# Optimization experiments

Measured on AMD Instinct MI355X. Metric: run time of the kernel, lower is better.

## Reference

```python
import jax, jax.numpy as jnp
import numpy as np
from jax import lax

H = 1024
NH = 16
R = 32
B, S = 32, 1024
LN_EPS = 1e-5

def _gelu(x):
    return jax.nn.gelu(x, approximate=False)

def setup_inputs() -> dict:
    key = jax.random.key(0)
    ks = jax.random.split(key, 24)
    w = lambda k, shape: jax.random.normal(k, shape, jnp.float32) * 0.02
    d = {}
    d['computation_results'] = jax.random.normal(ks[0], (B, S, H), jnp.float32)
    d['max_steps'] = 16
    # rule selector: Linear(H,H), GELU, Linear(H,R)
    d['rule_w1'] = w(ks[1], (H, H)); d['rule_b1'] = jnp.zeros((H,))
    d['rule_w2'] = w(ks[2], (R, H)); d['rule_b2'] = jnp.zeros((R,))
    d['rule_emb'] = jax.random.normal(ks[3], (R, H), jnp.float32)
    # MultiheadAttention packed in-proj [3H,H] and out-proj [H,H]
    d['attn_in_w'] = w(ks[4], (3 * H, H)); d['attn_in_b'] = jnp.zeros((3 * H,))
    d['attn_out_w'] = w(ks[5], (H, H)); d['attn_out_b'] = jnp.zeros((H,))
    # 2-layer LSTM, PyTorch gate order i,f,g,o
    d['lstm_wih0'] = w(ks[6], (4 * H, H)); d['lstm_whh0'] = w(ks[7], (4 * H, H))
    d['lstm_bih0'] = jnp.zeros((4 * H,)); d['lstm_bhh0'] = jnp.zeros((4 * H,))
    d['lstm_wih1'] = w(ks[8], (4 * H, H)); d['lstm_whh1'] = w(ks[9], (4 * H, H))
    d['lstm_bih1'] = jnp.zeros((4 * H,)); d['lstm_bhh1'] = jnp.zeros((4 * H,))
    # step generator: Linear(H,2H), LayerNorm(2H), GELU, Linear(2H,H)
    d['gen_w1'] = w(ks[10], (2 * H, H)); d['gen_b1'] = jnp.zeros((2 * H,))
    d['gen_ln_g'] = jnp.ones((2 * H,)); d['gen_ln_b'] = jnp.zeros((2 * H,))
    d['gen_w2'] = w(ks[11], (H, 2 * H)); d['gen_b2'] = jnp.zeros((H,))
    # step validator: Linear(2H,H), GELU, Linear(H,1), Sigmoid
    d['val_w1'] = w(ks[12], (H, 2 * H)); d['val_b1'] = jnp.zeros((H,))
    d['val_w2'] = w(ks[13], (1, H)); d['val_b2'] = jnp.zeros((1,))
    # proof verifier: Linear(H,H), GELU, Linear(H,1), Sigmoid
    d['ver_w1'] = w(ks[14], (H, H)); d['ver_b1'] = jnp.zeros((H,))
    d['ver_w2'] = w(ks[15], (1, H)); d['ver_b2'] = jnp.zeros((1,))
    return d


def reference(computation_results, max_steps, rule_w1, rule_b1, rule_w2, rule_b2, rule_emb,
              attn_in_w, attn_in_b, attn_out_w, attn_out_b,
              lstm_wih0, lstm_whh0, lstm_bih0, lstm_bhh0,
              lstm_wih1, lstm_whh1, lstm_bih1, lstm_bhh1,
              gen_w1, gen_b1, gen_ln_g, gen_ln_b, gen_w2, gen_b2,
              val_w1, val_b1, val_w2, val_b2,
              ver_w1, ver_b1, ver_w2, ver_b2):
    comp = computation_results
    b, s, h = comp.shape
    dh = h // NH
    scale = dh ** -0.5
    wq, wk, wv = jnp.split(attn_in_w, 3, axis=0)
    bq, bk, bv = jnp.split(attn_in_b, 3, axis=0)
    # K/V projections of the static context, computed once outside the step loop
    K = (comp @ wk.T + bk).reshape(b, s, NH, dh)  # [B,S,NH,dh]
    V = (comp @ wv.T + bv).reshape(b, s, NH, dh)
    lstm_params = ((lstm_wih0, lstm_whh0, lstm_bih0, lstm_bhh0),
                   (lstm_wih1, lstm_whh1, lstm_bih1, lstm_bhh1))

    def step(carry, _):
        ps, hmem, cmem = carry  # ps: [B,H]; hmem/cmem: [2,B,H]
        # rule selection
        logits = _gelu(ps @ rule_w1.T + rule_b1) @ rule_w2.T + rule_b2
        probs = jax.nn.softmax(logits, axis=-1)  # [B,R]
        sel = probs @ rule_emb  # [B,H]
        # single-query multi-head attention over computation context
        q = (ps @ wq.T + bq).reshape(b, NH, dh) * scale
        scores = jnp.einsum('bhd,bshd->bhs', q, K)
        a = jax.nn.softmax(scores, axis=-1)  # [B,NH,S]
        ctx = jnp.einsum('bhs,bshd->bhd', a, V).reshape(b, h) @ attn_out_w.T + attn_out_b
        attn_avg = a.mean(axis=1)  # head-averaged weights, [B,S]
        # 2-layer LSTM cell, one timestep
        x = ps
        hs, cs = [], []
        for l, (wih, whh, bih, bhh) in enumerate(lstm_params):
            g = x @ wih.T + bih + hmem[l] @ whh.T + bhh
            gi, gf, gg, go = jnp.split(g, 4, axis=-1)
            cn = jax.nn.sigmoid(gf) * cmem[l] + jax.nn.sigmoid(gi) * jnp.tanh(gg)
            hn = jax.nn.sigmoid(go) * jnp.tanh(cn)
            hs.append(hn); cs.append(cn); x = hn
        mem_out = x
        # step generator with LayerNorm+GELU
        si = ps + sel + ctx + mem_out
        z = si @ gen_w1.T + gen_b1
        mu = z.mean(axis=-1, keepdims=True)
        var = ((z - mu) ** 2).mean(axis=-1, keepdims=True)
        z = (z - mu) / jnp.sqrt(var + LN_EPS) * gen_ln_g + gen_ln_b
        nxt = _gelu(z) @ gen_w2.T + gen_b2
        val = jax.nn.sigmoid(_gelu(jnp.concatenate([ps, nxt], axis=-1) @ val_w1.T + val_b1) @ val_w2.T + val_b2)
        return (nxt, jnp.stack(hs), jnp.stack(cs)), (nxt, probs, val, attn_avg)

    init_state = comp[:, 0, :]
    carry0 = (init_state, jnp.zeros((2, b, h), comp.dtype), jnp.zeros((2, b, h), comp.dtype))
    (final, _, _), (steps, probs, vals, attn) = lax.scan(step, carry0, None, length=int(max_steps))
    proof_steps = jnp.concatenate([init_state[None], steps], axis=0)  # [T+1,B,H]
    proof_validity = jax.nn.sigmoid(_gelu(final @ ver_w1.T + ver_b1) @ ver_w2.T + ver_b2)  # [B,1]
    return proof_steps, proof_validity, probs, vals, attn
```

## Files before the change

### kernel.cpp

```cpp
#include <hip/hip_runtime.h>

typedef unsigned short u16;
typedef unsigned int u32;
typedef __attribute__((ext_vector_type(8))) short short8v;
typedef __attribute__((ext_vector_type(4))) float f32x4;

#define MFMA16(a,b,c) __builtin_amdgcn_mfma_f32_16x16x32_bf16((a),(b),(c),0,0,0)

__device__ __forceinline__ u16 f2bf(float f){
  u32 u = __float_as_uint(f);
  return (u16)((u + 0x7fffu + ((u >> 16) & 1u)) >> 16);
}
__device__ __forceinline__ float bf2f(u16 h){ return __uint_as_float(((u32)h) << 16); }
__device__ __forceinline__ float gelu_f(float x){ return 0.5f * x * (1.f + erff(x * 0.70710678118654752f)); }
__device__ __forceinline__ float sigm_f(float x){ return 1.f / (1.f + __expf(-x)); }
__device__ __forceinline__ void acc4(float4& a, const float4 b){ a.x+=b.x; a.y+=b.y; a.z+=b.z; a.w+=b.w; }

__device__ __forceinline__ void gl16(const void* g, void* l){
  __builtin_amdgcn_global_load_lds((const __attribute__((address_space(1))) u32*)g,
                                   (__attribute__((address_space(3))) u32*)l, 16, 0, 0);
}

struct CastJobs { const float* s[13]; u16* d[13]; int start[14]; };
__global__ __launch_bounds__(256) void cast_all_k(CastJobs J){
  int bx = blockIdx.x, j = 0;
  #pragma unroll
  for (int t = 0; t < 13; t++) if (bx >= J.start[t + 1]) j = t + 1;
  int i = (bx - J.start[j]) * 1024 + threadIdx.x * 4;
  float4 v = *(const float4*)(J.s[j] + i);
  ushort4 o; o.x = f2bf(v.x); o.y = f2bf(v.y); o.z = f2bf(v.z); o.w = f2bf(v.w);
  *(ushort4*)(J.d[j] + i) = o;
}

__global__ __launch_bounds__(256) void tcast_k(const float* __restrict__ s, u16* __restrict__ d){
  __shared__ float tile[32][33];
  int bx = blockIdx.x & 31, by = blockIdx.x >> 5;
  int tx = threadIdx.x & 31, ty = threadIdx.x >> 5;
  #pragma unroll
  for (int i = 0; i < 4; i++)
    tile[ty + i * 8][tx] = s[(size_t)(by * 32 + ty + i * 8) * 1024 + bx * 32 + tx];
  __syncthreads();
  #pragma unroll
  for (int i = 0; i < 4; i++)
    d[(size_t)(bx * 32 + ty + i * 8) * 1024 + by * 32 + tx] = f2bf(tile[tx][ty + i * 8]);
}

__global__ __launch_bounds__(256) void bias2_k(const float* __restrict__ gw1, const float* __restrict__ aob,
                                               const float* __restrict__ gb1, float* __restrict__ out){
  int j = blockIdx.x * 32 + (threadIdx.x >> 3);
  int l8 = threadIdx.x & 7;
  const float* r = gw1 + (size_t)j * 1024;
  float acc = 0.f;
  #pragma unroll 8
  for (int kk = 0; kk < 32; kk++){
    int k = kk * 32 + l8 * 4;
    float4 a = *(const float4*)(r + k);
    float4 w = *(const float4*)(aob + k);
    acc += a.x * w.x + a.y * w.y + a.z * w.z + a.w * w.w;
  }
  acc += __shfl_xor(acc, 1); acc += __shfl_xor(acc, 2); acc += __shfl_xor(acc, 4);
  if (l8 == 0) out[j] = gb1[j] + acc;
}

__global__ __launch_bounds__(256) void init_k(const float* __restrict__ comp, float* psa, float* psbz,
                                              float* outp, float* h0, float* c0, float* h1, float* c1){
  int i = blockIdx.x * 256 + threadIdx.x;
  int b = i >> 10, hh = i & 1023;
  float v = comp[(size_t)b * 1048576 + hh];
  psa[i] = v; psbz[i] = 0.f; outp[i] = v;
  h0[i] = 0.f; c0[i] = 0.f; h1[i] = 0.f; c1[i] = 0.f;
}

__global__ __launch_bounds__(256) void gemmkv_k(const u16* __restrict__ compb,
    const u16* __restrict__ Wk, const u16* __restrict__ Wv,
    const float* __restrict__ bk, const float* __restrict__ bv,
    u16* __restrict__ Kt, u16* __restrict__ Vb)
{
  __shared__ u16 Sh[16384];
  u16* As = Sh;
  u16* Bs = Sh + 8192;
  int tid = threadIdx.x;
  int x = blockIdx.x;
  int xcd = x & 7, p = x >> 3;
  int cpanel = xcd * 32 + (p >> 3);
  int wpanel = p & 7;
  int isK = (blockIdx.z != 0);
  const u16 *msrc, *nsrc; int m0, n0;
  if (!isK){ m0 = cpanel * 128; n0 = wpanel * 128; msrc = compb; nsrc = Wv; }
  else     { m0 = wpanel * 128; n0 = cpanel * 128; msrc = Wk;    nsrc = compb; }

  int w = tid >> 6, l = tid & 63, lr = l & 15, lk = l >> 4;
  int wm = (w >> 1) * 64, wn = (w & 1) * 64;
  f32x4 acc[4][4];
  #pragma unroll
  for (int i = 0; i < 4; i++)
    #pragma unroll
    for (int j = 0; j < 4; j++) acc[i][j] = (f32x4){0.f,0.f,0.f,0.f};

  for (int kc = 0; kc < 1024; kc += 64){
    #pragma unroll
    for (int r = 0; r < 4; r++){
      int s = tid + r * 256;
      int row = s >> 3, pp = s & 7;
      int lg = pp ^ (row & 7);
      gl16(msrc + (size_t)(m0 + row) * 1024 + kc + lg * 8, As + s * 8);
      gl16(nsrc + (size_t)(n0 + row) * 1024 + kc + lg * 8, Bs + s * 8);
    }
    __syncthreads();
    #pragma unroll
    for (int kk = 0; kk < 2; kk++){
      short8v a[4], bb[4];
      #pragma unroll
      for (int mi = 0; mi < 4; mi++){
        int row = wm + mi * 16 + lr;
        int ph = (kk * 4 + lk) ^ (row & 7);
        a[mi] = *(const short8v*)(As + row * 64 + ph * 8);
      }
      #pragma unroll
      for (int ni = 0; ni < 4; ni++){
        int row = wn + ni * 16 + lr;
        int ph = (kk * 4 + lk) ^ (row & 7);
        bb[ni] = *(const short8v*)(Bs + row * 64 + ph * 8);
      }
      #pragma unroll
      for (int mi = 0; mi < 4; mi++)
        #pragma unroll
        for (int ni = 0; ni < 4; ni++)
          acc[mi][ni] = MFMA16(a[mi], bb[ni], acc[mi][ni]);
    }
    __syncthreads();
  }
  #pragma unroll
  for (int mi = 0; mi < 4; mi++)
    #pragma unroll
    for (int ni = 0; ni < 4; ni++)
      #pragma unroll
      for (int r = 0; r < 4; r++){
        int row = wm + mi * 16 + lk * 4 + r;
        int col = wn + ni * 16 + lr;
        float bias = isK ? bk[m0 + row] : bv[n0 + col];
        Sh[row * 128 + col] = f2bf(acc[mi][ni][r] + bias);
      }
  __syncthreads();
  for (int i = tid; i < 2048; i += 256){
    int r = i >> 4, c8 = (i & 15) * 8;
    uint4 o = *(const uint4*)(Sh + r * 128 + c8);
    if (!isK){
      int bs = m0 + r, hd = n0 + c8;
      int b = bs >> 10, s = bs & 1023;
      int h = hd >> 6, d = hd & 63;
      *(uint4*)(Vb + ((size_t)(b * 16 + h) * 1024 + s) * 64 + d) = o;
    } else {
      int hd = m0 + r, bs = n0 + c8;
      int b = bs >> 10, s = bs & 1023;
      *(uint4*)(Kt + ((size_t)b * 1024 + hd) * 1024 + s) = o;
    }
  }
}

__global__ __launch_bounds__(256) void gemmbb_k(const u16* __restrict__ A, const u16* __restrict__ B,
                                                u16* __restrict__ C)
{
  __shared__ u16 As[128 * 64];
  __shared__ u16 Bs[128 * 64];
  int tid = threadIdx.x;
  int m0 = blockIdx.x * 128, n0 = blockIdx.y * 128;
  int w = tid >> 6, l = tid & 63, lr = l & 15, lk = l >> 4;
  int wm = (w >> 1) * 64, wn = (w & 1) * 64;
  f32x4 acc[4][4];
  #pragma unroll
  for (int i = 0; i < 4; i++)
    #pragma unroll
    for (int j = 0; j < 4; j++) acc[i][j] = (f32x4){0.f,0.f,0.f,0.f};
  for (int kc = 0; kc < 1024; kc += 64){
    #pragma unroll
    for (int r = 0; r < 4; r++){
      int s = tid + r * 256;
      int row = s >> 3, pp = s & 7;
      int lg = pp ^ (row & 7);
      gl16(A + (size_t)(m0 + row) * 1024 + kc + lg * 8, As + s * 8);
      gl16(B + (size_t)(n0 + row) * 1024 + kc + lg * 8, Bs + s * 8);
    }
    __syncthreads();
    #pragma unroll
    for (int kk = 0; kk < 2; kk++){
      short8v a[4], bb[4];
      #pragma unroll
      for (int mi = 0; mi < 4; mi++){
        int row = wm + mi * 16 + lr;
        int ph = (kk * 4 + lk) ^ (row & 7);
        a[mi] = *(const short8v*)(As + row * 64 + ph * 8);
      }
      #pragma unroll
      for (int ni = 0; ni < 4; ni++){
        int row = wn + ni * 16 + lr;
        int ph = (kk * 4 + lk) ^ (row & 7);
        bb[ni] = *(const short8v*)(Bs + row * 64 + ph * 8);
      }
      #pragma unroll
      for (int mi = 0; mi < 4; mi++)
        #pragma unroll
        for (int ni = 0; ni < 4; ni++)
          acc[mi][ni] = MFMA16(a[mi], bb[ni], acc[mi][ni]);
    }
    __syncthreads();
  }
  #pragma unroll
  for (int mi = 0; mi < 4; mi++)
    #pragma unroll
    for (int ni = 0; ni < 4; ni++)
      #pragma unroll
      for (int r = 0; r < 4; r++){
        int row = m0 + wm + mi * 16 + lk * 4 + r;
        int col = n0 + wn + ni * 16 + lr;
        C[(size_t)row * 1024 + col] = f2bf(acc[mi][ni][r]);
      }
}

struct LinSeg {
  const float* X0; const float* Xa; const float* Xb; const float* Xc;
  const u16* W1; const float* b1;
  const float* Y; const u16* W2; const float* b2;
  float* out; float* out2;
  int K1, ldx, ld1, K2, ld2, N, act, gate;
  float scale;
  float* stats;
  const float* lng; const float* lnb; const float* lnstats;
  const float* cprev; float* cout; float* hout;
};

__device__ __forceinline__ short8v pack8(float4 v0, float4 v1){
  short8v r;
  r[0]=(short)f2bf(v0.x); r[1]=(short)f2bf(v0.y); r[2]=(short)f2bf(v0.z); r[3]=(short)f2bf(v0.w);
  r[4]=(short)f2bf(v1.x); r[5]=(short)f2bf(v1.y); r[6]=(short)f2bf(v1.z); r[7]=(short)f2bf(v1.w);
  return r;
}

__device__ __forceinline__ short8v load_sum8(const LinSeg& S, int row, int kb){
  size_t o = (size_t)row * S.ldx + kb;
  float4 v0 = *(const float4*)(S.X0 + o);
  float4 v1 = *(const float4*)(S.X0 + o + 4);
  if (S.lng){
    float mu = S.lnstats[row] * (1.f / 2048.f);
    float ms = S.lnstats[32 + row] * (1.f / 2048.f);
    float rstd = rsqrtf(ms - mu * mu + 1e-5f);
    float4 g0 = *(const float4*)(S.lng + kb), g1 = *(const float4*)(S.lng + kb + 4);
    float4 b0 = *(const float4*)(S.lnb + kb), b1 = *(const float4*)(S.lnb + kb + 4);
    v0.x = gelu_f((v0.x - mu) * rstd * g0.x + b0.x);
    v0.y = gelu_f((v0.y - mu) * rstd * g0.y + b0.y);
    v0.z = gelu_f((v0.z - mu) * rstd * g0.z + b0.z);
    v0.w = gelu_f((v0.w - mu) * rstd * g0.w + b0.w);
    v1.x = gelu_f((v1.x - mu) * rstd * g1.x + b1.x);
    v1.y = gelu_f((v1.y - mu) * rstd * g1.y + b1.y);
    v1.z = gelu_f((v1.z - mu) * rstd * g1.z + b1.z);
    v1.w = gelu_f((v1.w - mu) * rstd * g1.w + b1.w);
  } else {
    if (S.Xa){ acc4(v0, *(const float4*)(S.Xa + o)); acc4(v1, *(const float4*)(S.Xa + o + 4)); }
    if (S.Xb){ acc4(v0, *(const float4*)(S.Xb + o)); acc4(v1, *(const float4*)(S.Xb + o + 4)); }
    if (S.Xc){ acc4(v0, *(const float4*)(S.Xc + o)); acc4(v1, *(const float4*)(S.Xc + o + 4)); }
  }
  return pack8(v0, v1);
}
__device__ __forceinline__ short8v load_y8(const float* p){
  return pack8(*(const float4*)(p), *(const float4*)(p + 4));
}

typedef float Red16[32][16];

__device__ void lin_body(const LinSeg& S, int bi, int tid, Red16* red){
  int c0 = bi * 16, j0 = bi * 4;
  int w = tid >> 6, l = tid & 63, lr = l & 15, lk = l >> 4;
  int wc0 = S.gate ? ((lr >> 2) << 10) + j0 + (lr & 3) : c0 + lr;
  f32x4 acc[2];
  acc[0] = (f32x4){0.f,0.f,0.f,0.f};
  acc[1] = (f32x4){0.f,0.f,0.f,0.f};

  {
    int chunk = S.K1 >> 2;
    int kb0 = w * chunk + lk * 8;
    for (int kk = 0; kk < chunk; kk += 32){
      int kb = kb0 + kk;
      short8v a0 = load_sum8(S, lr, kb);
      short8v a1 = load_sum8(S, lr + 16, kb);
      short8v w0 = *(const short8v*)(S.W1 + (size_t)wc0 * S.ld1 + kb);
      acc[0] = MFMA16(a0, w0, acc[0]);
      acc[1] = MFMA16(a1, w0, acc[1]);
    }
  }
  if (S.Y){
    int chunk = S.K2 >> 2;
    int kb0 = w * chunk + lk * 8;
    for (int kk = 0; kk < chunk; kk += 32){
      int kb = kb0 + kk;
      short8v a0 = load_y8(S.Y + (size_t)lr * S.K2 + kb);
      short8v a1 = load_y8(S.Y + (size_t)(lr + 16) * S.K2 + kb);
      short8v w0 = *(const short8v*)(S.W2 + (size_t)wc0 * S.ld2 + kb);
      acc[0] = MFMA16(a0, w0, acc[0]);
      acc[1] = MFMA16(a1, w0, acc[1]);
    }
  }
  #pragma unroll
  for (int mi = 0; mi < 2; mi++)
    #pragma unroll
    for (int r = 0; r < 4; r++)
      red[w][mi * 16 + lk * 4 + r][lr] = acc[mi][r];
  __syncthreads();
  if (S.gate){
    if (tid < 128){
      int row = tid >> 2, j = tid & 3;
      float s[4];
      #pragma unroll
      for (int g = 0; g < 4; g++){
        float v = 0.f;
        #pragma unroll
        for (int ww = 0; ww < 4; ww++) v += red[ww][row][g * 4 + j];
        s[g] = v;
      }
      int gc = j0 + j;
      float gI = s[0] + S.b1[gc]        + S.b2[gc];
      float gF = s[1] + S.b1[1024 + gc] + S.b2[1024 + gc];
      float gG = s[2] + S.b1[2048 + gc] + S.b2[2048 + gc];
      float gO = s[3] + S.b1[3072 + gc] + S.b2[3072 + gc];
      int idx = row * 1024 + gc;
      float cN = sigm_f(gF) * S.cprev[idx] + sigm_f(gI) * tanhf(gG);
      S.cout[idx] = cN;
      S.hout[idx] = sigm_f(gO) * tanhf(cN);
    }
    return;
  }
  float vout[2]; int iout[2];
  int cnt = 0;
  for (int i = tid; i < 512; i += 256){
    int row = i >> 4, col = i & 15;
    float v = 0.f;
    #pragma unroll
    for (int ww = 0; ww < 4; ww++) v += red[ww][row][col];
    if (S.b1) v += S.b1[c0 + col];
    if (S.b2) v += S.b2[c0 + col];
    if (S.act == 1) v = gelu_f(v);
    else if (S.act == 2) v *= S.scale;
    S.out[(size_t)row * S.N + c0 + col] = v;
    if (S.out2) S.out2[(size_t)row * S.N + c0 + col] = v;
    vout[cnt] = v; iout[cnt] = i; cnt++;
  }
  if (S.stats){
    __syncthreads();
    float* rf = (float*)red;
    rf[iout[0]] = vout[0]; rf[512 + iout[0]] = vout[0] * vout[0];
    rf[iout[1]] = vout[1]; rf[512 + iout[1]] = vout[1] * vout[1];
// ... 62 lines not shown
    u32 vv = vp[s * 32];
    float w = scp[s];
    c0 += w * bf2f((u16)(vv & 0xffff));
    c1 += w * bf2f((u16)(vv >> 16));
  }
  *(float2*)(ctxp + chunk * 64 + dd2 * 2) = make_float2(c0, c1);
  __syncthreads();
  if (tid < 64){
    float r = 0.f;
    #pragma unroll
    for (int c = 0; c < 8; c++) r += ctxp[c * 64 + tid];
    ctx0[bh * 64 + tid] = r;
  }
}

__device__ void rule2_job(int b, int tid, const float* h1a, const float* w2, const float* b2,
                          const float* emb, float* probs_out, float* sel, float* shf){
  float* lg = shf;
  float* psh = shf + 32;
  int j = tid >> 3, l8 = tid & 7;
  const float* xr = h1a + b * 1024;
  const float* wr = w2 + j * 1024;
  float acc = 0.f;
  #pragma unroll 8
  for (int kk = 0; kk < 32; kk++){
    int k = kk * 32 + l8 * 4;
    float4 xv = *(const float4*)(xr + k);
    float4 wv = *(const float4*)(wr + k);
    acc += xv.x * wv.x + xv.y * wv.y + xv.z * wv.z + xv.w * wv.w;
  }
  acc += __shfl_xor(acc, 1); acc += __shfl_xor(acc, 2); acc += __shfl_xor(acc, 4);
  if (l8 == 0) lg[j] = acc + b2[j];
  __syncthreads();
  if (tid < 32){
    float v = lg[tid];
    float m = v;
    for (int o = 1; o < 32; o <<= 1) m = fmaxf(m, __shfl_xor(m, o));
    float e = __expf(v - m);
    float s = e;
    for (int o = 1; o < 32; o <<= 1) s += __shfl_xor(s, o);
    float p = e / s;
    psh[tid] = p;
    probs_out[b * 32 + tid] = p;
  }
  __syncthreads();
  for (int j2 = tid; j2 < 1024; j2 += 256){
    float a2 = 0.f;
    #pragma unroll
    for (int r = 0; r < 32; r++) a2 += psh[r] * emb[r * 1024 + j2];
    sel[b * 1024 + j2] = a2;
  }
}

__global__ __launch_bounds__(256) void step_d1_k(LinSeg sRule, LinSeg sQ, LinSeg sL0,
                                                 const float* pa, const float* pb, float* proof_t){
  __shared__ float red[4][32][16];
  int bx = blockIdx.x, tid = threadIdx.x;
  if (bx < 64){ lin_body(sRule, bx, tid, red); return; }
  if (bx < 128){ lin_body(sQ, bx - 64, tid, red); return; }
  if (bx < 384){ lin_body(sL0, bx - 128, tid, red); return; }
  int i = (bx - 384) * 1024 + tid * 4;
  float4 va = *(const float4*)(pa + i);
  float4 vb = *(const float4*)(pb + i);
  acc4(va, vb);
  *(float4*)(proof_t + i) = va;
}

struct D2Params {
  const float* qbuf;
  const u16* Kt; const u16* Vb; float* afull; float* ctx0;
  const float* h1a; const float* w2; const float* b2r; const float* emb;
  float* probs_out; float* sel;
  LinSeg sL1; float* lnstats;
};
__global__ __launch_bounds__(256) void step_d2_k(D2Params P){
  __shared__ float red[4][32][16];
  float* shf = &red[0][0][0];
  int bx = blockIdx.x, tid = threadIdx.x;
  if (bx < 512){ attn_job(bx, tid, P.qbuf, P.Kt, P.Vb, P.afull, P.ctx0, shf); return; }
  if (bx < 544){ rule2_job(bx - 512, tid, P.h1a, P.w2, P.b2r, P.emb, P.probs_out, P.sel, shf); return; }
  if (bx < 800){ lin_body(P.sL1, bx - 544, tid, red); return; }
  if (tid < 64) P.lnstats[tid] = 0.f;
}

__global__ __launch_bounds__(256) void fixup_k(const float* __restrict__ pa, const float* __restrict__ pb,
                                               float* __restrict__ out){
  int i = blockIdx.x * 1024 + threadIdx.x * 4;
  float4 va = *(const float4*)(pa + i);
  float4 vb = *(const float4*)(pb + i);
  acc4(va, vb);
  *(float4*)(out + i) = va;
}

__global__ __launch_bounds__(256) void valver_k(const u16* __restrict__ vw1, const float* __restrict__ vb1,
    const u16* __restrict__ verw1, const float* __restrict__ verb1,
    const float* __restrict__ proof, const float* __restrict__ pfa, const float* __restrict__ pfb,
    float* __restrict__ v1){
  __shared__ float red[4][32][16];
  int t = blockIdx.y;
  LinSeg S = {};
  if (t < 16){
    S.X0 = proof + (size_t)t * 32768; S.K1 = 1024; S.ldx = 1024; S.W1 = vw1; S.ld1 = 2048; S.b1 = vb1;
    S.Y = proof + (size_t)(t + 1) * 32768; S.K2 = 1024; S.W2 = vw1 + 1024; S.ld2 = 2048;
  } else {
    S.X0 = pfa; S.Xa = pfb; S.K1 = 1024; S.ldx = 1024; S.W1 = verw1; S.ld1 = 1024; S.b1 = verb1;
  }
  S.out = v1 + (size_t)t * 32768; S.N = 1024; S.act = 1;
  lin_body(S, blockIdx.x, threadIdx.x, red);
}

__global__ __launch_bounds__(256) void dotsig_b_k(const float* __restrict__ v1,
    const float* __restrict__ w2v, const float* __restrict__ b2v,
    const float* __restrict__ w2ver, const float* __restrict__ b2ver,
    float* __restrict__ out_vals, float* __restrict__ out_valid){
  int t = blockIdx.x;
  const float* w = (t < 16) ? w2v : w2ver;
  const float* bs = (t < 16) ? b2v : b2ver;
  const float* x = v1 + (size_t)t * 32768;
  int b = threadIdx.x >> 3, l8 = threadIdx.x & 7;
  const float* xr = x + (size_t)b * 1024;
  float acc = 0.f;
  #pragma unroll 8
  for (int kk = 0; kk < 32; kk++){
    int k = kk * 32 + l8 * 4;
    float4 xv = *(const float4*)(xr + k);
    float4 wv = *(const float4*)(w + k);
    acc += xv.x * wv.x + xv.y * wv.y + xv.z * wv.z + xv.w * wv.w;
  }
  acc += __shfl_xor(acc, 1); acc += __shfl_xor(acc, 2); acc += __shfl_xor(acc, 4);
  if (l8 == 0){
    float r = sigm_f(acc + bs[0]);
    if (t < 16) out_vals[t * 32 + b] = r; else out_valid[b] = r;
  }
}

__global__ __launch_bounds__(256) void attnavg_all_k(const float* __restrict__ afull, float* __restrict__ out){
  int idx = blockIdx.x * 256 + threadIdx.x;
  int t = idx >> 15, r = idx & 32767;
  int b = r >> 10, s = r & 1023;
  const float* base = afull + (size_t)t * 524288 + (size_t)b * 16384;
  float acc = 0.f;
  #pragma unroll
  for (int h = 0; h < 16; h++) acc += base[h * 1024 + s];
  out[idx] = acc * (1.f / 16.f);
}

extern "C" void kernel_launch(void* const* d_in, const int* in_sizes, int n_in,
                              void* d_out, int out_size, void* d_ws, size_t ws_size,
                              hipStream_t stream) {
  const float* comp      = (const float*)d_in[0];
  const float* rule_w1   = (const float*)d_in[2];
  const float* rule_b1   = (const float*)d_in[3];
  const float* rule_w2   = (const float*)d_in[4];
  const float* rule_b2   = (const float*)d_in[5];
  const float* rule_emb  = (const float*)d_in[6];
  const float* attn_in_w = (const float*)d_in[7];
  const float* attn_in_b = (const float*)d_in[8];
  const float* attn_out_w= (const float*)d_in[9];
  const float* attn_out_b= (const float*)d_in[10];
  const float* wih0 = (const float*)d_in[11];
  const float* whh0 = (const float*)d_in[12];
  const float* bih0 = (const float*)d_in[13];
  const float* bhh0 = (const float*)d_in[14];
  const float* wih1 = (const float*)d_in[15];
  const float* whh1 = (const float*)d_in[16];
  const float* bih1 = (const float*)d_in[17];
  const float* bhh1 = (const float*)d_in[18];
  const float* gen_w1 = (const float*)d_in[19];
  const float* gen_b1 = (const float*)d_in[20];
  const float* ln_g   = (const float*)d_in[21];
  const float* ln_b   = (const float*)d_in[22];
  const float* gen_w2 = (const float*)d_in[23];
  const float* gen_b2 = (const float*)d_in[24];
  const float* val_w1 = (const float*)d_in[25];
  const float* val_b1 = (const float*)d_in[26];
  const float* val_w2 = (const float*)d_in[27];
  const float* val_b2 = (const float*)d_in[28];
  const float* ver_w1 = (const float*)d_in[29];
  const float* ver_b1 = (const float*)d_in[30];
  const float* ver_w2 = (const float*)d_in[31];
  const float* ver_b2 = (const float*)d_in[32];

  float* out_f     = (float*)d_out;
  float* out_proof = out_f;
  float* out_valid = out_f + 17 * 32768;
  float* out_probs = out_valid + 32;
  float* out_vals  = out_probs + 16 * 1024;
  float* out_attn  = out_vals + 16 * 32;

  char* wp = (char*)d_ws;
  auto carve = [&](size_t bytes) -> void* {
    void* p = (void*)wp; wp += (bytes + 255) & ~(size_t)255; return p;
  };
  u16* Kt    = (u16*)carve((size_t)33554432 * 2);
  u16* Vb    = (u16*)carve((size_t)33554432 * 2);
  u16* compb = (u16*)carve((size_t)33554432 * 2);
  float* afull_all = (float*)compb;
  u16* rw1b  = (u16*)carve(2097152);
  u16* wqb   = (u16*)carve(2097152);
  u16* wkb   = (u16*)carve(2097152);
  u16* wvb   = (u16*)carve(2097152);
  u16* aowTb = (u16*)carve(2097152);
  u16* wih0b = (u16*)carve(8388608);
  u16* whh0b = (u16*)carve(8388608);
  u16* wih1b = (u16*)carve(8388608);
  u16* whh1b = (u16*)carve(8388608);
  u16* gw1b  = (u16*)carve(4194304);
  u16* gw2b  = (u16*)carve(4194304);
  u16* vw1b  = (u16*)carve(4194304);
  u16* verw1b= (u16*)carve(2097152);
  u16* gaw   = (u16*)carve(4194304);
  float* bias2 = (float*)carve(8192);
  float* psa[2] = { (float*)carve(131072), (float*)carve(131072) };
  float* psq[2] = { (float*)carve(131072), (float*)carve(131072) };
  float* h0b[2] = { (float*)carve(131072), (float*)carve(131072) };
  float* c0b[2] = { (float*)carve(131072), (float*)carve(131072) };
  float* h1b[2] = { (float*)carve(131072), (float*)carve(131072) };
  float* c1b[2] = { (float*)carve(131072), (float*)carve(131072) };
  float* h1act = (float*)carve(131072);
  float* sel   = (float*)carve(131072);
  float* qbuf  = (float*)carve(131072);
  float* ctx0  = (float*)carve(131072);
  float* zbuf  = (float*)carve(262144);
  float* v1buf = (float*)carve(2228224);
  float* lnstats = (float*)carve(256);
  (void)ws_size; (void)in_sizes; (void)n_in; (void)out_size;

  CastJobs J;
  const float* srcs[13] = { rule_w1, attn_in_w, attn_in_w + 1048576, attn_in_w + 2097152,
                            wih0, whh0, wih1, whh1, gen_w1, gen_w2, val_w1, ver_w1, comp };
  u16* dsts[13] = { rw1b, wqb, wkb, wvb, wih0b, whh0b, wih1b, whh1b, gw1b, gw2b, vw1b, verw1b, compb };
  int sizes[13] = { 1048576, 1048576, 1048576, 1048576,
                    4194304, 4194304, 4194304, 4194304, 2097152, 2097152, 2097152, 1048576, 33554432 };
  int st = 0;
  for (int i = 0; i < 13; i++){ J.s[i] = srcs[i]; J.d[i] = dsts[i]; J.start[i] = st; st += sizes[i] / 1024; }
  J.start[13] = st;
  cast_all_k<<<dim3(st), dim3(256), 0, stream>>>(J);
  tcast_k<<<dim3(1024), dim3(256), 0, stream>>>(attn_out_w, aowTb);

  gemmkv_k<<<dim3(2048, 1, 2), dim3(256), 0, stream>>>(compb, wkb, wvb,
      attn_in_b + 1024, attn_in_b + 2048, Kt, Vb);
  gemmbb_k<<<dim3(16, 8), dim3(256), 0, stream>>>(gw1b, aowTb, gaw);
  bias2_k<<<dim3(64), dim3(256), 0, stream>>>(gen_w1, attn_out_b, gen_b1, bias2);

  init_k<<<dim3(128), dim3(256), 0, stream>>>(comp, psa[0], psq[0], out_proof,
      h0b[0], c0b[0], h1b[0], c1b[0]);

  for (int t = 0; t < 16; t++){
    int cur = t & 1, nx = cur ^ 1;
    float* pa = psa[cur];
    float* pb = psq[cur];
    float* afull_t = afull_all + (size_t)t * 524288;
    LinSeg sRule = {}; sRule.X0 = pa; sRule.Xa = pb; sRule.K1 = 1024; sRule.ldx = 1024;
    sRule.W1 = rw1b; sRule.ld1 = 1024; sRule.b1 = rule_b1; sRule.out = h1act; sRule.N = 1024; sRule.act = 1;
    LinSeg sQ = {}; sQ.X0 = pa; sQ.Xa = pb; sQ.K1 = 1024; sQ.ldx = 1024;
    sQ.W1 = wqb; sQ.ld1 = 1024; sQ.b1 = attn_in_b; sQ.out = qbuf; sQ.N = 1024; sQ.act = 2; sQ.scale = 0.125f;
    LinSeg sL0 = {}; sL0.X0 = pa; sL0.Xa = pb; sL0.K1 = 1024; sL0.ldx = 1024;
    sL0.W1 = wih0b; sL0.ld1 = 1024; sL0.b1 = bih0;
    sL0.Y = h0b[cur]; sL0.K2 = 1024; sL0.W2 = whh0b; sL0.ld2 = 1024; sL0.b2 = bhh0;
    sL0.gate = 1; sL0.cprev = c0b[cur]; sL0.cout = c0b[nx]; sL0.hout = h0b[nx];
    step_d1_k<<<dim3(416), dim3(256), 0, stream>>>(sRule, sQ, sL0, pa, pb,
        out_proof + (size_t)t * 32768);
    D2Params P;
    P.qbuf = qbuf; P.Kt = Kt; P.Vb = Vb; P.afull = afull_t; P.ctx0 = ctx0;
    P.h1a = h1act; P.w2 = rule_w2; P.b2r = rule_b2; P.emb = rule_emb;
    P.probs_out = out_probs + t * 1024; P.sel = sel;
    LinSeg sL1 = {}; sL1.X0 = h0b[nx]; sL1.K1 = 1024; sL1.ldx = 1024;
    sL1.W1 = wih1b; sL1.ld1 = 1024; sL1.b1 = bih1;
    sL1.Y = h1b[cur]; sL1.K2 = 1024; sL1.W2 = whh1b; sL1.ld2 = 1024; sL1.b2 = bhh1;
    sL1.gate = 1; sL1.cprev = c1b[cur]; sL1.cout = c1b[nx]; sL1.hout = h1b[nx];
    P.sL1 = sL1; P.lnstats = lnstats;
    step_d2_k<<<dim3(801), dim3(256), 0, stream>>>(P);
    LinSeg sG1 = {}; sG1.X0 = pa; sG1.Xa = pb; sG1.Xb = sel; sG1.Xc = h1b[nx];
    sG1.K1 = 1024; sG1.ldx = 1024; sG1.W1 = gw1b; sG1.ld1 = 1024; sG1.b1 = bias2;
    sG1.Y = ctx0; sG1.K2 = 1024; sG1.W2 = gaw; sG1.ld2 = 1024;
    sG1.out = zbuf; sG1.N = 2048; sG1.stats = lnstats;
    linmulti_k<<<dim3(128), dim3(256), 0, stream>>>(sG1, sG1, sG1, 128, 0);
    LinSeg sA = {}; sA.X0 = zbuf; sA.K1 = 1024; sA.ldx = 2048;
    sA.W1 = gw2b; sA.ld1 = 2048; sA.b1 = gen_b2;
    sA.lng = ln_g; sA.lnb = ln_b; sA.lnstats = lnstats;
    sA.out = psa[nx]; sA.N = 1024;
    LinSeg sB = {}; sB.X0 = zbuf + 1024; sB.K1 = 1024; sB.ldx = 2048;
    sB.W1 = gw2b + 1024; sB.ld1 = 2048;
    sB.lng = ln_g + 1024; sB.lnb = ln_b + 1024; sB.lnstats = lnstats;
    sB.out = psq[nx]; sB.N = 1024;
    linmulti_k<<<dim3(128), dim3(256), 0, stream>>>(sA, sB, sB, 64, 64);
  }
  fixup_k<<<dim3(32), dim3(256), 0, stream>>>(psa[0], psq[0], out_proof + (size_t)16 * 32768);
  valver_k<<<dim3(64, 17), dim3(256), 0, stream>>>(vw1b, val_b1, verw1b, ver_b1,
      out_proof, psa[0], psq[0], v1buf);
  dotsig_b_k<<<dim3(17), dim3(256), 0, stream>>>(v1buf, val_w2, val_b2, ver_w2, ver_b2,
      out_vals, out_valid);
  attnavg_all_k<<<dim3(2048), dim3(256), 0, stream>>>(afull_all, out_attn);
}
```

Measured before the change: 2.019 ms.

## Fold generator output projection into next-step consumer weights to drop a launch per step

Precomputes fused weight products (rule_w1·gen_w2, Wq·gen_w2, Wih0·gen_w2, gen_w1·gen_w2) and folded biases once, so each step's consumers read the LayerNorm+GELU activations of the previous step directly with K=2048. This removes the separate gen_w2 linear launch per step; the proof-step output is produced inside step_d1 instead. The trade is doubled K for several per-step GEMVs plus extra precompute GEMMs and the precision risk of bf16-rounded fused weights.

New measurement: 2.439 ms. 1.21x slower.

```diff
diff --git a/kernel.cpp b/kernel.cpp
--- a/kernel.cpp
+++ b/kernel.cpp
@@ -45,29 +45,109 @@
     d[(size_t)(bx * 32 + ty + i * 8) * 1024 + by * 32 + tx] = f2bf(tile[tx][ty + i * 8]);
 }
 
-__global__ __launch_bounds__(256) void bias2_k(const float* __restrict__ gw1, const float* __restrict__ aob,
-                                               const float* __restrict__ gb1, float* __restrict__ out){
-  int j = blockIdx.x * 32 + (threadIdx.x >> 3);
+__global__ __launch_bounds__(256) void ttcast_k(const float* __restrict__ s, u16* __restrict__ d){
+  __shared__ float tile[32][33];
+  int cx = blockIdx.x & 63, ry = blockIdx.x >> 6;
+  int tx = threadIdx.x & 31, ty = threadIdx.x >> 5;
+  #pragma unroll
+  for (int i = 0; i < 4; i++)
+    tile[ty + i * 8][tx] = s[(size_t)(ry * 32 + ty + i * 8) * 2048 + cx * 32 + tx];
+  __syncthreads();
+  #pragma unroll
+  for (int i = 0; i < 4; i++)
+    d[(size_t)(cx * 32 + ty + i * 8) * 1024 + ry * 32 + tx] = f2bf(tile[tx][ty + i * 8]);
+}
+
+struct GJobs { const u16* A[5]; const u16* B[5]; u16* C[5]; int mb[5]; int nb[5]; int ldc[5]; };
+__global__ __launch_bounds__(256) void gemmbb_k(GJobs J){
+  int z = blockIdx.z;
+  if ((int)blockIdx.x >= J.mb[z] || (int)blockIdx.y >= J.nb[z]) return;
+  const u16* A = J.A[z]; const u16* B = J.B[z]; u16* C = J.C[z]; int ldc = J.ldc[z];
+  __shared__ u16 As[128 * 64];
+  __shared__ u16 Bs[128 * 64];
+  int tid = threadIdx.x;
+  int m0 = blockIdx.x * 128, n0 = blockIdx.y * 128;
+  int w = tid >> 6, l = tid & 63, lr = l & 15, lk = l >> 4;
+  int wm = (w >> 1) * 64, wn = (w & 1) * 64;
+  f32x4 acc[4][4];
+  #pragma unroll
+  for (int i = 0; i < 4; i++)
+    #pragma unroll
+    for (int j = 0; j < 4; j++) acc[i][j] = (f32x4){0.f,0.f,0.f,0.f};
+  for (int kc = 0; kc < 1024; kc += 64){
+    #pragma unroll
+    for (int r = 0; r < 4; r++){
+      int s = tid + r * 256;
+      int row = s >> 3, pp = s & 7;
+      int lg = pp ^ (row & 7);
+      gl16(A + (size_t)(m0 + row) * 1024 + kc + lg * 8, As + s * 8);
+      gl16(B + (size_t)(n0 + row) * 1024 + kc + lg * 8, Bs + s * 8);
+    }
+    __syncthreads();
+    #pragma unroll
+    for (int kk = 0; kk < 2; kk++){
+      short8v a[4], bb[4];
+      #pragma unroll
+      for (int mi = 0; mi < 4; mi++){
+        int row = wm + mi * 16 + lr;
+        int ph = (kk * 4 + lk) ^ (row & 7);
+        a[mi] = *(const short8v*)(As + row * 64 + ph * 8);
+      }
+      #pragma unroll
+      for (int ni = 0; ni < 4; ni++){
+        int row = wn + ni * 16 + lr;
+        int ph = (kk * 4 + lk) ^ (row & 7);
+        bb[ni] = *(const short8v*)(Bs + row * 64 + ph * 8);
+      }
+      #pragma unroll
+      for (int mi = 0; mi < 4; mi++)
+        #pragma unroll
+        for (int ni = 0; ni < 4; ni++)
+          acc[mi][ni] = MFMA16(a[mi], bb[ni], acc[mi][ni]);
+    }
+    __syncthreads();
+  }
+  #pragma unroll
+  for (int mi = 0; mi < 4; mi++)
+    #pragma unroll
+    for (int ni = 0; ni < 4; ni++)
+      #pragma unroll
+      for (int r = 0; r < 4; r++){
+        int row = m0 + wm + mi * 16 + lk * 4 + r;
+        int col = n0 + wn + ni * 16 + lr;
+        C[(size_t)row * ldc + col] = f2bf(acc[mi][ni][r]);
+      }
+}
+
+struct BJobs { const float* W[5]; const float* v[5]; const float* v2[5];
+               const float* base[5]; float* out[5]; int start[6]; };
+__global__ __launch_bounds__(256) void biasfold_k(BJobs J){
+  int bx = blockIdx.x, j = 0;
+  #pragma unroll
+  for (int t = 0; t < 5; t++) if (bx >= J.start[t + 1]) j = t + 1;
+  int row = (bx - J.start[j]) * 32 + (threadIdx.x >> 3);
   int l8 = threadIdx.x & 7;
-  const float* r = gw1 + (size_t)j * 1024;
+  const float* wr = J.W[j] + (size_t)row * 1024;
+  const float* v = J.v[j]; const float* v2 = J.v2[j];
   float acc = 0.f;
   #pragma unroll 8
   for (int kk = 0; kk < 32; kk++){
     int k = kk * 32 + l8 * 4;
-    float4 a = *(const float4*)(r + k);
-    float4 w = *(const float4*)(aob + k);
-    acc += a.x * w.x + a.y * w.y + a.z * w.z + a.w * w.w;
+    float4 wv = *(const float4*)(wr + k);
+    float4 a = *(const float4*)(v + k);
+    if (v2) acc4(a, *(const float4*)(v2 + k));
+    acc += wv.x * a.x + wv.y * a.y + wv.z * a.z + wv.w * a.w;
   }
   acc += __shfl_xor(acc, 1); acc += __shfl_xor(acc, 2); acc += __shfl_xor(acc, 4);
-  if (l8 == 0) out[j] = gb1[j] + acc;
-}
-
-__global__ __launch_bounds__(256) void init_k(const float* __restrict__ comp, float* psa, float* psbz,
+  if (l8 == 0) J.out[j][row] = J.base[j][row] + acc;
+}
+
+__global__ __launch_bounds__(256) void init_k(const float* __restrict__ comp, float* ps0,
                                               float* outp, float* h0, float* c0, float* h1, float* c1){
   int i = blockIdx.x * 256 + threadIdx.x;
   int b = i >> 10, hh = i & 1023;
   float v = comp[(size_t)b * 1048576 + hh];
-  psa[i] = v; psbz[i] = 0.f; outp[i] = v;
+  ps0[i] = v; outp[i] = v;
   h0[i] = 0.f; c0[i] = 0.f; h1[i] = 0.f; c1[i] = 0.f;
 }
 
@@ -158,74 +238,16 @@
   }
 }
 
-__global__ __launch_bounds__(256) void gemmbb_k(const u16* __restrict__ A, const u16* __restrict__ B,
-                                                u16* __restrict__ C)
-{
-  __shared__ u16 As[128 * 64];
-  __shared__ u16 Bs[128 * 64];
-  int tid = threadIdx.x;
-  int m0 = blockIdx.x * 128, n0 = blockIdx.y * 128;
-  int w = tid >> 6, l = tid & 63, lr = l & 15, lk = l >> 4;
-  int wm = (w >> 1) * 64, wn = (w & 1) * 64;
-  f32x4 acc[4][4];
-  #pragma unroll
-  for (int i = 0; i < 4; i++)
-    #pragma unroll
-    for (int j = 0; j < 4; j++) acc[i][j] = (f32x4){0.f,0.f,0.f,0.f};
-  for (int kc = 0; kc < 1024; kc += 64){
-    #pragma unroll
-    for (int r = 0; r < 4; r++){
-      int s = tid + r * 256;
-      int row = s >> 3, pp = s & 7;
-      int lg = pp ^ (row & 7);
-      gl16(A + (size_t)(m0 + row) * 1024 + kc + lg * 8, As + s * 8);
-      gl16(B + (size_t)(n0 + row) * 1024 + kc + lg * 8, Bs + s * 8);
-    }
-    __syncthreads();
-    #pragma unroll
-    for (int kk = 0; kk < 2; kk++){
-      short8v a[4], bb[4];
-      #pragma unroll
-      for (int mi = 0; mi < 4; mi++){
-        int row = wm + mi * 16 + lr;
-        int ph = (kk * 4 + lk) ^ (row & 7);
-        a[mi] = *(const short8v*)(As + row * 64 + ph * 8);
-      }
-      #pragma unroll
-      for (int ni = 0; ni < 4; ni++){
-        int row = wn + ni * 16 + lr;
-        int ph = (kk * 4 + lk) ^ (row & 7);
-        bb[ni] = *(const short8v*)(Bs + row * 64 + ph * 8);
-      }
-      #pragma unroll
-      for (int mi = 0; mi < 4; mi++)
-        #pragma unroll
-        for (int ni = 0; ni < 4; ni++)
-          acc[mi][ni] = MFMA16(a[mi], bb[ni], acc[mi][ni]);
-    }
-    __syncthreads();
-  }
-  #pragma unroll
-  for (int mi = 0; mi < 4; mi++)
-    #pragma unroll
-    for (int ni = 0; ni < 4; ni++)
-      #pragma unroll
-      for (int r = 0; r < 4; r++){
-        int row = m0 + wm + mi * 16 + lk * 4 + r;
-        int col = n0 + wn + ni * 16 + lr;
-        C[(size_t)row * 1024 + col] = f2bf(acc[mi][ni][r]);
-      }
-}
-
 struct LinSeg {
   const float* X0; const float* Xa; const float* Xb; const float* Xc;
-  const u16* W1; const float* b1;
-  const float* Y; const u16* W2; const float* b2;
-  float* out; float* out2;
-  int K1, ldx, ld1, K2, ld2, N, act, gate;
+  const u16* W1; int K1, ldx, ld1;
+  const float* Y; const u16* W2; int K2, ld2;
+  const float* Zp; const u16* WZ; int KZ, ldz, ldwz;
+  const float* lng; const float* lnb; const float* lnstats;
+  const float* b1; const float* b2;
+  float* out; float* out2; int N, act, gate;
   float scale;
   float* stats;
-  const float* lng; const float* lnb; const float* lnstats;
   const float* cprev; float* cout; float* hout;
 };
 
@@ -240,29 +262,32 @@
   size_t o = (size_t)row * S.ldx + kb;
   float4 v0 = *(const float4*)(S.X0 + o);
   float4 v1 = *(const float4*)(S.X0 + o + 4);
-  if (S.lng){
-    float mu = S.lnstats[row] * (1.f / 2048.f);
-    float ms = S.lnstats[32 + row] * (1.f / 2048.f);
-    float rstd = rsqrtf(ms - mu * mu + 1e-5f);
-    float4 g0 = *(const float4*)(S.lng + kb), g1 = *(const float4*)(S.lng + kb + 4);
-    float4 b0 = *(const float4*)(S.lnb + kb), b1 = *(const float4*)(S.lnb + kb + 4);
-    v0.x = gelu_f((v0.x - mu) * rstd * g0.x + b0.x);
-    v0.y = gelu_f((v0.y - mu) * rstd * g0.y + b0.y);
-    v0.z = gelu_f((v0.z - mu) * rstd * g0.z + b0.z);
-    v0.w = gelu_f((v0.w - mu) * rstd * g0.w + b0.w);
-    v1.x = gelu_f((v1.x - mu) * rstd * g1.x + b1.x);
-    v1.y = gelu_f((v1.y - mu) * rstd * g1.y + b1.y);
-    v1.z = gelu_f((v1.z - mu) * rstd * g1.z + b1.z);
-    v1.w = gelu_f((v1.w - mu) * rstd * g1.w + b1.w);
-  } else {
-    if (S.Xa){ acc4(v0, *(const float4*)(S.Xa + o)); acc4(v1, *(const float4*)(S.Xa + o + 4)); }
-    if (S.Xb){ acc4(v0, *(const float4*)(S.Xb + o)); acc4(v1, *(const float4*)(S.Xb + o + 4)); }
-    if (S.Xc){ acc4(v0, *(const float4*)(S.Xc + o)); acc4(v1, *(const float4*)(S.Xc + o + 4)); }
-  }
+  if (S.Xa){ acc4(v0, *(const float4*)(S.Xa + o)); acc4(v1, *(const float4*)(S.Xa + o + 4)); }
+  if (S.Xb){ acc4(v0, *(const float4*)(S.Xb + o)); acc4(v1, *(const float4*)(S.Xb + o + 4)); }
+  if (S.Xc){ acc4(v0, *(const float4*)(S.Xc + o)); acc4(v1, *(const float4*)(S.Xc + o + 4)); }
   return pack8(v0, v1);
 }
 __device__ __forceinline__ short8v load_y8(const float* p){
   return pack8(*(const float4*)(p), *(const float4*)(p + 4));
+}
+__device__ __forceinline__ short8v load_z8(const LinSeg& S, int row, int kb){
+  size_t o = (size_t)row * S.ldz + kb;
+  float4 v0 = *(const float4*)(S.Zp + o);
+  float4 v1 = *(const float4*)(S.Zp + o + 4);
+  float mu = S.lnstats[row] * (1.f / 2048.f);
+  float ms = S.lnstats[32 + row] * (1.f / 2048.f);
+  float rstd = rsqrtf(ms - mu * mu + 1e-5f);
+  float4 g0 = *(const float4*)(S.lng + kb), g1 = *(const float4*)(S.lng + kb + 4);
+  float4 b0 = *(const float4*)(S.lnb + kb), b1 = *(const float4*)(S.lnb + kb + 4);
+  v0.x = gelu_f((v0.x - mu) * rstd * g0.x + b0.x);
+  v0.y = gelu_f((v0.y - mu) * rstd * g0.y + b0.y);
+  v0.z = gelu_f((v0.z - mu) * rstd * g0.z + b0.z);
+  v0.w = gelu_f((v0.w - mu) * rstd * g0.w + b0.w);
+  v1.x = gelu_f((v1.x - mu) * rstd * g1.x + b1.x);
+  v1.y = gelu_f((v1.y - mu) * rstd * g1.y + b1.y);
+  v1.z = gelu_f((v1.z - mu) * rstd * g1.z + b1.z);
+  v1.w = gelu_f((v1.w - mu) * rstd * g1.w + b1.w);
+  return pack8(v0, v1);
 }
 
 typedef float Red16[32][16];
@@ -275,7 +300,7 @@
   acc[0] = (f32x4){0.f,0.f,0.f,0.f};
   acc[1] = (f32x4){0.f,0.f,0.f,0.f};
 
-  {
+  if (S.X0){
     int chunk = S.K1 >> 2;
     int kb0 = w * chunk + lk * 8;
     for (int kk = 0; kk < chunk; kk += 32){
@@ -295,6 +320,18 @@
       short8v a0 = load_y8(S.Y + (size_t)lr * S.K2 + kb);
       short8v a1 = load_y8(S.Y + (size_t)(lr + 16) * S.K2 + kb);
       short8v w0 = *(const short8v*)(S.W2 + (size_t)wc0 * S.ld2 + kb);
+      acc[0] = MFMA16(a0, w0, acc[0]);
+      acc[1] = MFMA16(a1, w0, acc[1]);
+    }
+  }
+  if (S.Zp){
+    int chunk = S.KZ >> 2;
+    int kb0 = w * chunk + lk * 8;
+    for (int kk = 0; kk < chunk; kk += 32){
+      int kb = kb0 + kk;
+      short8v a0 = load_z8(S, lr, kb);
+      short8v a1 = load_z8(S, lr + 16, kb);
+      short8v w0 = *(const short8v*)(S.WZ + (size_t)wc0 * S.ldwz + kb);
       acc[0] = MFMA16(a0, w0, acc[0]);
       acc[1] = MFMA16(a1, w0, acc[1]);
     }
@@ -463,18 +500,13 @@
   }
 }
 
-__global__ __launch_bounds__(256) void step_d1_k(LinSeg sRule, LinSeg sQ, LinSeg sL0,
-                                                 const float* pa, const float* pb, float* proof_t){
+__global__ __launch_bounds__(256) void step_d1_k(LinSeg sRule, LinSeg sQ, LinSeg sL0, LinSeg sPs){
   __shared__ float red[4][32][16];
   int bx = blockIdx.x, tid = threadIdx.x;
   if (bx < 64){ lin_body(sRule, bx, tid, red); return; }
   if (bx < 128){ lin_body(sQ, bx - 64, tid, red); return; }
   if (bx < 384){ lin_body(sL0, bx - 128, tid, red); return; }
-  int i = (bx - 384) * 1024 + tid * 4;
-  float4 va = *(const float4*)(pa + i);
-  float4 vb = *(const float4*)(pb + i);
-  acc4(va, vb);
-  *(float4*)(proof_t + i) = va;
+  lin_body(sPs, bx - 384, tid, red);
 }
 
 struct D2Params {
@@ -494,19 +526,9 @@
   if (tid < 64) P.lnstats[tid] = 0.f;
 }
 
-__global__ __launch_bounds__(256) void fixup_k(const float* __restrict__ pa, const float* __restrict__ pb,
-                                               float* __restrict__ out){
-  int i = blockIdx.x * 1024 + threadIdx.x * 4;
-  float4 va = *(const float4*)(pa + i);
-  float4 vb = *(const float4*)(pb + i);
-  acc4(va, vb);
-  *(float4*)(out + i) = va;
-}
-
 __global__ __launch_bounds__(256) void valver_k(const u16* __restrict__ vw1, const float* __restrict__ vb1,
     const u16* __restrict__ verw1, const float* __restrict__ verb1,
-    const float* __restrict__ proof, const float* __restrict__ pfa, const float* __restrict__ pfb,
-    float* __restrict__ v1){
+    const float* __restrict__ proof, float* __restrict__ v1){
   __shared__ float red[4][32][16];
   int t = blockIdx.y;
   LinSeg S = {};
@@ -514,7 +536,7 @@
     S.X0 = proof + (size_t)t * 32768; S.K1 = 1024; S.ldx = 1024; S.W1 = vw1; S.ld1 = 2048; S.b1 = vb1;
     S.Y = proof + (size_t)(t + 1) * 32768; S.K2 = 1024; S.W2 = vw1 + 1024; S.ld2 = 2048;
   } else {
-    S.X0 = pfa; S.Xa = pfb; S.K1 = 1024; S.ldx = 1024; S.W1 = verw1; S.ld1 = 1024; S.b1 = verb1;
+    S.X0 = proof + (size_t)16 * 32768; S.K1 = 1024; S.ldx = 1024; S.W1 = verw1; S.ld1 = 1024; S.b1 = verb1;
   }
   S.out = v1 + (size_t)t * 32768; S.N = 1024; S.act = 1;
   lin_body(S, blockIdx.x, threadIdx.x, red);
@@ -607,6 +629,11 @@
   u16* Vb    = (u16*)carve((size_t)33554432 * 2);
   u16* compb = (u16*)carve((size_t)33554432 * 2);
   float* afull_all = (float*)compb;
+  char* chi  = (char*)compb + 33554432;
+  u16* gw2T  = (u16*)chi;
+  u16* rwg   = (u16*)(chi + 4194304);
+  u16* wqg   = (u16*)(chi + 8388608);
+  u16* wih0g = (u16*)(chi + 12582912);
   u16* rw1b  = (u16*)carve(2097152);
   u16* wqb   = (u16*)carve(2097152);
   u16* wkb   = (u16*)carve(2097152);
@@ -621,20 +648,24 @@
   u16* vw1b  = (u16*)carve(4194304);
   u16* verw1b= (u16*)carve(2097152);
   u16* gaw   = (u16*)carve(4194304);
-  float* bias2 = (float*)carve(8192);
-  float* psa[2] = { (float*)carve(131072), (float*)carve(131072) };
-  float* psq[2] = { (float*)carve(131072), (float*)carve(131072) };
+  u16* g1g   = (u16*)carve(8388608);
+  float* brl   = (float*)carve(4096);
+  float* bqg   = (float*)carve(4096);
+  float* bih0g = (float*)carve(16384);
+  float* b2t0  = (float*)carve(8192);
+  float* b2tn  = (float*)carve(8192);
+  float* ps0   = (float*)carve(131072);
   float* h0b[2] = { (float*)carve(131072), (float*)carve(131072) };
   float* c0b[2] = { (float*)carve(131072), (float*)carve(131072) };
   float* h1b[2] = { (float*)carve(131072), (float*)carve(131072) };
   float* c1b[2] = { (float*)carve(131072), (float*)carve(131072) };
+  float* zb[2]  = { (float*)carve(262144), (float*)carve(262144) };
+  float* lnst[2]= { (float*)carve(256), (float*)carve(256) };
   float* h1act = (float*)carve(131072);
   float* sel   = (float*)carve(131072);
   float* qbuf  = (float*)carve(131072);
   float* ctx0  = (float*)carve(131072);
-  float* zbuf  = (float*)carve(262144);
   float* v1buf = (float*)carve(2228224);
-  float* lnstats = (float*)carve(256);
   (void)ws_size; (void)in_sizes; (void)n_in; (void)out_size;
 
   CastJobs J;
@@ -651,27 +682,54 @@
 
   gemmkv_k<<<dim3(2048, 1, 2), dim3(256), 0, stream>>>(compb, wkb, wvb,
       attn_in_b + 1024, attn_in_b + 2048, Kt, Vb);
-  gemmbb_k<<<dim3(16, 8), dim3(256), 0, stream>>>(gw1b, aowTb, gaw);
-  bias2_k<<<dim3(64), dim3(256), 0, stream>>>(gen_w1, attn_out_b, gen_b1, bias2);
-
-  init_k<<<dim3(128), dim3(256), 0, stream>>>(comp, psa[0], psq[0], out_proof,
+
+  ttcast_k<<<dim3(2048), dim3(256), 0, stream>>>(gen_w2, gw2T);
+  GJobs G;
+  G.A[0]=rw1b;  G.B[0]=gw2T;  G.C[0]=rwg;   G.mb[0]=8;  G.nb[0]=16; G.ldc[0]=2048;
+  G.A[1]=wqb;   G.B[1]=gw2T;  G.C[1]=wqg;   G.mb[1]=8;  G.nb[1]=16; G.ldc[1]=2048;
+  G.A[2]=wih0b; G.B[2]=gw2T;  G.C[2]=wih0g; G.mb[2]=32; G.nb[2]=16; G.ldc[2]=2048;
+  G.A[3]=gw1b;  G.B[3]=gw2T;  G.C[3]=g1g;   G.mb[3]=16; G.nb[3]=16; G.ldc[3]=2048;
+  G.A[4]=gw1b;  G.B[4]=aowTb; G.C[4]=gaw;   G.mb[4]=16; G.nb[4]=8;  G.ldc[4]=1024;
+  gemmbb_k<<<dim3(32, 16, 5), dim3(256), 0, stream>>>(G);
+
+  BJobs B;
+  B.W[0]=rule_w1;  B.v[0]=gen_b2;     B.v2[0]=nullptr; B.base[0]=rule_b1;   B.out[0]=brl;
+  B.W[1]=attn_in_w;B.v[1]=gen_b2;     B.v2[1]=nullptr; B.base[1]=attn_in_b; B.out[1]=bqg;
+  B.W[2]=wih0;     B.v[2]=gen_b2;     B.v2[2]=nullptr; B.base[2]=bih0;      B.out[2]=bih0g;
+  B.W[3]=gen_w1;   B.v[3]=attn_out_b; B.v2[3]=nullptr; B.base[3]=gen_b1;    B.out[3]=b2t0;
+  B.W[4]=gen_w1;   B.v[4]=attn_out_b; B.v2[4]=gen_b2;  B.base[4]=gen_b1;    B.out[4]=b2tn;
+  B.start[0]=0; B.start[1]=32; B.start[2]=64; B.start[3]=192; B.start[4]=256; B.start[5]=320;
+  biasfold_k<<<dim3(320), dim3(256), 0, stream>>>(B);
+
+  init_k<<<dim3(128), dim3(256), 0, stream>>>(comp, ps0, out_proof,
       h0b[0], c0b[0], h1b[0], c1b[0]);
 
   for (int t = 0; t < 16; t++){
     int cur = t & 1, nx = cur ^ 1;
-    float* pa = psa[cur];
-    float* pb = psq[cur];
+    int p = nx;
     float* afull_t = afull_all + (size_t)t * 524288;
-    LinSeg sRule = {}; sRule.X0 = pa; sRule.Xa = pb; sRule.K1 = 1024; sRule.ldx = 1024;
-    sRule.W1 = rw1b; sRule.ld1 = 1024; sRule.b1 = rule_b1; sRule.out = h1act; sRule.N = 1024; sRule.act = 1;
-    LinSeg sQ = {}; sQ.X0 = pa; sQ.Xa = pb; sQ.K1 = 1024; sQ.ldx = 1024;
-    sQ.W1 = wqb; sQ.ld1 = 1024; sQ.b1 = attn_in_b; sQ.out = qbuf; sQ.N = 1024; sQ.act = 2; sQ.scale = 0.125f;
-    LinSeg sL0 = {}; sL0.X0 = pa; sL0.Xa = pb; sL0.K1 = 1024; sL0.ldx = 1024;
-    sL0.W1 = wih0b; sL0.ld1 = 1024; sL0.b1 = bih0;
+    LinSeg sRule = {}, sQ = {}, sL0 = {}, sPs = {};
+    if (t == 0){
+      sRule.X0 = ps0; sRule.K1 = 1024; sRule.ldx = 1024; sRule.W1 = rw1b; sRule.ld1 = 1024;
+      sRule.b1 = rule_b1;
+      sQ.X0 = ps0; sQ.K1 = 1024; sQ.ldx = 1024; sQ.W1 = wqb; sQ.ld1 = 1024; sQ.b1 = attn_in_b;
+      sL0.X0 = ps0; sL0.K1 = 1024; sL0.ldx = 1024; sL0.W1 = wih0b; sL0.ld1 = 1024; sL0.b1 = bih0;
+    } else {
+      sRule.Zp = zb[p]; sRule.KZ = 2048; sRule.ldz = 2048; sRule.WZ = rwg; sRule.ldwz = 2048;
+      sRule.lng = ln_g; sRule.lnb = ln_b; sRule.lnstats = lnst[p]; sRule.b1 = brl;
+      sQ.Zp = zb[p]; sQ.KZ = 2048; sQ.ldz = 2048; sQ.WZ = wqg; sQ.ldwz = 2048;
+      sQ.lng = ln_g; sQ.lnb = ln_b; sQ.lnstats = lnst[p]; sQ.b1 = bqg;
+      sL0.Zp = zb[p]; sL0.KZ = 2048; sL0.ldz = 2048; sL0.WZ = wih0g; sL0.ldwz = 2048;
+      sL0.lng = ln_g; sL0.lnb = ln_b; sL0.lnstats = lnst[p]; sL0.b1 = bih0g;
+      sPs.Zp = zb[p]; sPs.KZ = 2048; sPs.ldz = 2048; sPs.WZ = gw2b; sPs.ldwz = 2048;
+      sPs.lng = ln_g; sPs.lnb = ln_b; sPs.lnstats = lnst[p]; sPs.b1 = gen_b2;
+      sPs.out = out_proof + (size_t)t * 32768; sPs.N = 1024;
+    }
+    sRule.out = h1act; sRule.N = 1024; sRule.act = 1;
+    sQ.out = qbuf; sQ.N = 1024; sQ.act = 2; sQ.scale = 0.125f;
     sL0.Y = h0b[cur]; sL0.K2 = 1024; sL0.W2 = whh0b; sL0.ld2 = 1024; sL0.b2 = bhh0;
     sL0.gate = 1; sL0.cprev = c0b[cur]; sL0.cout = c0b[nx]; sL0.hout = h0b[nx];
-    step_d1_k<<<dim3(416), dim3(256), 0, stream>>>(sRule, sQ, sL0, pa, pb,
-        out_proof + (size_t)t * 32768);
+    step_d1_k<<<dim3(t ? 448 : 384), dim3(256), 0, stream>>>(sRule, sQ, sL0, sPs);
     D2Params P;
     P.qbuf = qbuf; P.Kt = Kt; P.Vb = Vb; P.afull = afull_t; P.ctx0 = ctx0;
     P.h1a = h1act; P.w2 = rule_w2; P.b2r = rule_b2; P.emb = rule_emb;
@@ -680,26 +738,27 @@
     sL1.W1 = wih1b; sL1.ld1 = 1024; sL1.b1 = bih1;
     sL1.Y = h1b[cur]; sL1.K2 = 1024; sL1.W2 = whh1b; sL1.ld2 = 1024; sL1.b2 = bhh1;
     sL1.gate = 1; sL1.cprev = c1b[cur]; sL1.cout = c1b[nx]; sL1.hout = h1b[nx];
-    P.sL1 = sL1; P.lnstats = lnstats;
+    P.sL1 = sL1; P.lnstats = lnst[cur];
     step_d2_k<<<dim3(801), dim3(256), 0, stream>>>(P);
-    LinSeg sG1 = {}; sG1.X0 = pa; sG1.Xa = pb; sG1.Xb = sel; sG1.Xc = h1b[nx];
-    sG1.K1 = 1024; sG1.ldx = 1024; sG1.W1 = gw1b; sG1.ld1 = 1024; sG1.b1 = bias2;
-    sG1.Y = ctx0; sG1.K2 = 1024; sG1.W2 = gaw; sG1.ld2 = 1024;
-    sG1.out = zbuf; sG1.N = 2048; sG1.stats = lnstats;
-    linmulti_k<<<dim3(128), dim3(256), 0, stream>>>(sG1, sG1, sG1, 128, 0);
-    LinSeg sA = {}; sA.X0 = zbuf; sA.K1 = 1024; sA.ldx = 2048;
-    sA.W1 = gw2b; sA.ld1 = 2048; sA.b1 = gen_b2;
-    sA.lng = ln_g; sA.lnb = ln_b; sA.lnstats = lnstats;
-    sA.out = psa[nx]; sA.N = 1024;
-    LinSeg sB = {}; sB.X0 = zbuf + 1024; sB.K1 = 1024; sB.ldx = 2048;
-    sB.W1 = gw2b + 1024; sB.ld1 = 2048;
-    sB.lng = ln_g + 1024; sB.lnb = ln_b + 1024; sB.lnstats = lnstats;
-    sB.out = psq[nx]; sB.N = 1024;
-    linmulti_k<<<dim3(128), dim3(256), 0, stream>>>(sA, sB, sB, 64, 64);
-  }
-  fixup_k<<<dim3(32), dim3(256), 0, stream>>>(psa[0], psq[0], out_proof + (size_t)16 * 32768);
-  valver_k<<<dim3(64, 17), dim3(256), 0, stream>>>(vw1b, val_b1, verw1b, ver_b1,
-      out_proof, psa[0], psq[0], v1buf);
+    LinSeg sG = {};
+    if (t == 0){
+      sG.X0 = ps0; sG.Xa = sel; sG.Xb = h1b[nx]; sG.b1 = b2t0;
+    } else {
+      sG.X0 = sel; sG.Xa = h1b[nx]; sG.b1 = b2tn;
+      sG.Zp = zb[p]; sG.KZ = 2048; sG.ldz = 2048; sG.WZ = g1g; sG.ldwz = 2048;
+      sG.lng = ln_g; sG.lnb = ln_b; sG.lnstats = lnst[p];
+    }
+    sG.K1 = 1024; sG.ldx = 1024; sG.W1 = gw1b; sG.ld1 = 1024;
+    sG.Y = ctx0; sG.K2 = 1024; sG.W2 = gaw; sG.ld2 = 1024;
+    sG.out = zb[cur]; sG.N = 2048; sG.stats = lnst[cur];
+    linmulti_k<<<dim3(128), dim3(256), 0, stream>>>(sG, sG, sG, 128, 0);
+  }
+  LinSeg sFin = {};
+  sFin.Zp = zb[1]; sFin.KZ = 2048; sFin.ldz = 2048; sFin.WZ = gw2b; sFin.ldwz = 2048;
+  sFin.lng = ln_g; sFin.lnb = ln_b; sFin.lnstats = lnst[1]; sFin.b1 = gen_b2;
+  sFin.out = out_proof + (size_t)16 * 32768; sFin.N = 1024;
+  linmulti_k<<<dim3(64), dim3(256), 0, stream>>>(sFin, sFin, sFin, 64, 0);
+  valver_k<<<dim3(64, 17), dim3(256), 0, stream>>>(vw1b, val_b1, verw1b, ver_b1, out_proof, v1buf);
   dotsig_b_k<<<dim3(17), dim3(256), 0, stream>>>(v1buf, val_w2, val_b2, ver_w2, ver_b2,
       out_vals, out_valid);
   attnavg_all_k<<<dim3(2048), dim3(256), 0, stream>>>(afull_all, out_attn);
```
